# Performance work log

Hardware: AMD Instinct MI355X
Metric: run time of the kernel (lower is better)

The kernel has to match this reference:

```python
import jax, jax.numpy as jnp
import numpy as np

B, NQ, NK = 4, 2048, 2048
D_MODEL, H, DK, DV, M = 512, 8, 64, 64, 40


def setup_inputs() -> dict:
    key = jax.random.key(0)
    ks = jax.random.split(key, 12)
    s = 0.02  # param init scale (stand-in for xavier)
    return {
        "queries": jax.random.normal(ks[0], (B, NQ, D_MODEL), jnp.float32),
        "keys": jax.random.normal(ks[1], (B, NK, D_MODEL), jnp.float32),
        "values": jax.random.normal(ks[2], (B, NK, D_MODEL), jnp.float32),
        "attention_weights": jax.random.uniform(ks[3], (B, H, NQ, NK), jnp.float32),
        "attention_mask": jax.random.randint(ks[4], (B, H, NQ, NK), 0, 2) == 1,
        "Wq": jax.random.normal(ks[5], (D_MODEL, H * DK), jnp.float32) * s,
        "bq": jnp.zeros((H * DK,), jnp.float32),
        "Wk": jax.random.normal(ks[6], (D_MODEL, H * DK), jnp.float32) * s,
        "bk": jnp.zeros((H * DK,), jnp.float32),
        "Wv": jax.random.normal(ks[7], (D_MODEL, H * DV), jnp.float32) * s,
        "bv": jnp.zeros((H * DV,), jnp.float32),
        "Wo": jax.random.normal(ks[8], (H * DV, D_MODEL), jnp.float32) * s,
        "bo": jnp.zeros((D_MODEL,), jnp.float32),
        "m_k": jax.random.normal(ks[9], (1, M, H * DK), jnp.float32) * s,
        "m_v": jax.random.normal(ks[10], (1, M, H * DV), jnp.float32) * s,
    }


def reference(queries, keys, values, attention_weights, attention_mask,
              Wq, bq, Wk, bk, Wv, bv, Wo, bo, m_k, m_v):
    b, nq, _ = queries.shape
    nk = keys.shape[1]
    # learned memory slots, scaled and broadcast over batch
    mk = jnp.sqrt(jnp.float32(DK)) * jnp.broadcast_to(m_k, (b, M, H * DK))
    mv = jnp.sqrt(jnp.float32(M)) * jnp.broadcast_to(m_v, (b, M, H * DV))
    q = (queries @ Wq + bq).reshape(b, nq, H, DK).transpose(0, 2, 1, 3)      # (b,h,nq,dk)
    k = jnp.concatenate([keys @ Wk + bk, mk], axis=1)
    k = k.reshape(b, nk + M, H, DK).transpose(0, 2, 3, 1)                     # (b,h,dk,nk+m)
    v = jnp.concatenate([values @ Wv + bv, mv], axis=1)
    v = v.reshape(b, nk + M, H, DV).transpose(0, 2, 1, 3)                     # (b,h,nk+m,dv)
    att = jnp.matmul(q, k) / jnp.sqrt(jnp.float32(DK))                        # (b,h,nq,nk+m)
    att_x = att[..., :nk] * attention_weights
    att_x = jnp.where(attention_mask, -jnp.inf, att_x)
    att = jnp.concatenate([att_x, att[..., nk:]], axis=-1)
    att = jax.nn.softmax(att, axis=-1)
    out = jnp.matmul(att, v).transpose(0, 2, 1, 3).reshape(b, nq, H * DV)
    return out @ Wo + bo
```

## Files before the change

kernel.cpp:

```cpp
#include <hip/hip_runtime.h>
#include <hip/hip_bf16.h>
#include <cstdint>
#include <cstddef>

typedef __bf16 bf16_t;
typedef __bf16 bf16x8 __attribute__((ext_vector_type(8)));
typedef __bf16 bf16x4 __attribute__((ext_vector_type(4)));
typedef float  f32x4  __attribute__((ext_vector_type(4)));

#define B_    4
#define NQ_   2048
#define NK_   2048
#define H_    8
#define MSL_  40
#define NKP_  2112
#define SCL2  0.18033688011112042f

#define GLOAD_LDS16(GP, LP)                                                        \
    __builtin_amdgcn_global_load_lds(                                              \
        (const __attribute__((address_space(1))) unsigned int*)(GP),               \
        (__attribute__((address_space(3))) unsigned int*)(LP), 16, 0, 0)

__global__ void detect_mask(const unsigned int* __restrict__ m, int* __restrict__ flag)
{
    __shared__ int found;
    if (threadIdx.x == 0) found = 0;
    __syncthreads();
    unsigned int acc = 0;
    for (int i = threadIdx.x; i < 65536; i += 256)
        acc |= (m[i] & 0xFFFFFF00u);
    if (acc) found = 1;
    __syncthreads();
    if (threadIdx.x == 0) *flag = found;
}

__global__ void transpose_convert4(const float* __restrict__ s0, const float* __restrict__ s1,
                                   const float* __restrict__ s2, const float* __restrict__ s3,
                                   bf16_t* __restrict__ d0, bf16_t* __restrict__ d1,
                                   bf16_t* __restrict__ d2, bf16_t* __restrict__ d3)
{
    const float* src; bf16_t* dst;
    switch (blockIdx.z) {
        case 0:  src = s0; dst = d0; break;
        case 1:  src = s1; dst = d1; break;
        case 2:  src = s2; dst = d2; break;
        default: src = s3; dst = d3; break;
    }
    __shared__ float t[32][33];
    int x  = blockIdx.x * 32 + threadIdx.x;
    int y0 = blockIdx.y * 32 + threadIdx.y;
#pragma unroll
    for (int i = 0; i < 32; i += 8)
        t[threadIdx.y + i][threadIdx.x] = src[(size_t)(y0 + i) * 512 + x];
    __syncthreads();
    int ox  = blockIdx.y * 32 + threadIdx.x;
    int oy0 = blockIdx.x * 32 + threadIdx.y;
#pragma unroll
    for (int i = 0; i < 32; i += 8)
        dst[(size_t)(oy0 + i) * 512 + ox] = (bf16_t)t[threadIdx.x][threadIdx.y + i];
}

__global__ void memfill(const float* __restrict__ m_k, const float* __restrict__ m_v,
                        bf16_t* __restrict__ Kbf, bf16_t* __restrict__ Vt)
{
    int tid = blockIdx.x * 256 + threadIdx.x;
    if (tid < 4 * 64 * 512) {
        int c  = tid & 511;
        int mi = (tid >> 9) & 63;
        int b  = tid >> 15;
        float v = (mi < MSL_) ? 8.0f * m_k[mi * 512 + c] : 0.0f;
        Kbf[((size_t)b * NKP_ + NK_ + mi) * 512 + c] = (bf16_t)v;
    } else {
        int t  = tid - 4 * 64 * 512;
        int mi = t & 63;
        int dv = (t >> 6) & 63;
        int h  = (t >> 12) & 7;
        int b  = t >> 15;
        float v = (mi < MSL_) ? 6.324555320336759f * m_v[mi * 512 + h * 64 + dv] : 0.0f;
        Vt[(((size_t)b * H_ + h) * 64 + dv) * NKP_ + NK_ + mi] = (bf16_t)v;
    }
}

template<bool AF32>
__device__ __forceinline__ void gemm_core(
    bf16_t (*As)[72], bf16_t (*Bs)[72],
    const void* __restrict__ Av, const bf16_t* __restrict__ BT,
    const float* __restrict__ bias, void* __restrict__ dstv,
    int dstBS, int epi, float scale)
{
    const int tid = threadIdx.x;
    const int w = tid >> 6, l = tid & 63, lg = l >> 4, lr = l & 15;
    const int wr = w >> 1, wc = w & 1;
    const int blockM = blockIdx.x * 128, blockN = blockIdx.y * 128;

    f32x4 acc[4][4];
    const f32x4 zv = {0.f, 0.f, 0.f, 0.f};
#pragma unroll
    for (int i = 0; i < 4; i++)
#pragma unroll
        for (int j = 0; j < 4; j++) acc[i][j] = zv;

    const int ar = tid >> 1;
    const int ac = (tid & 1) * 32;

    for (int k0 = 0; k0 < 512; k0 += 64) {
        if (k0) __syncthreads();
        if constexpr (AF32) {
            const float* arow = (const float*)Av + (size_t)(blockM + ar) * 512 + k0 + ac;
#pragma unroll
            for (int i = 0; i < 8; i++) {
                float4 v = ((const float4*)arow)[i];
                bf16x4 pk = {(bf16_t)v.x, (bf16_t)v.y, (bf16_t)v.z, (bf16_t)v.w};
                *(bf16x4*)&As[ar][ac + i * 4] = pk;
            }
        } else {
            const bf16_t* arow = (const bf16_t*)Av + (size_t)(blockM + ar) * 512 + k0 + ac;
#pragma unroll
            for (int i = 0; i < 4; i++)
                *(uint4*)&As[ar][ac + i * 8] = ((const uint4*)arow)[i];
        }
        {
            const bf16_t* brow = BT + (size_t)(blockN + ar) * 512 + k0 + ac;
#pragma unroll
            for (int i = 0; i < 4; i++)
                *(uint4*)&Bs[ar][ac + i * 8] = ((const uint4*)brow)[i];
        }
        __syncthreads();
#pragma unroll
        for (int ks = 0; ks < 2; ks++) {
            bf16x8 af[4], bfr[4];
#pragma unroll
            for (int mi = 0; mi < 4; mi++)
                af[mi] = *(const bf16x8*)&As[wr * 64 + mi * 16 + lr][ks * 32 + lg * 8];
#pragma unroll
            for (int ni = 0; ni < 4; ni++)
                bfr[ni] = *(const bf16x8*)&Bs[wc * 64 + ni * 16 + lr][ks * 32 + lg * 8];
#pragma unroll
            for (int mi = 0; mi < 4; mi++)
#pragma unroll
                for (int ni = 0; ni < 4; ni++)
                    acc[mi][ni] = __builtin_amdgcn_mfma_f32_16x16x32_bf16(af[mi], bfr[ni], acc[mi][ni], 0, 0, 0);
        }
    }

    const int colbase = blockN + wc * 64;
    float bias_v[4];
#pragma unroll
    for (int ni = 0; ni < 4; ni++) bias_v[ni] = bias[colbase + ni * 16 + lr];

#pragma unroll
    for (int mi = 0; mi < 4; mi++) {
        const int r0 = blockM + wr * 64 + mi * 16 + lg * 4;
#pragma unroll
        for (int ni = 0; ni < 4; ni++) {
            const int c = colbase + ni * 16 + lr;
            f32x4 v = acc[mi][ni];
            if (epi == 2) {
                float* dst = (float*)dstv;
#pragma unroll
                for (int j = 0; j < 4; j++)
                    dst[(size_t)(r0 + j) * 512 + c] = (v[j] + bias_v[ni]) * scale;
            } else if (epi == 0) {
                bf16_t* dst = (bf16_t*)dstv;
#pragma unroll
                for (int j = 0; j < 4; j++) {
                    int rr = r0 + j;
                    int bb = rr >> 11, nn = rr & 2047;
                    dst[((size_t)bb * dstBS + nn) * 512 + c] = (bf16_t)((v[j] + bias_v[ni]) * scale);
                }
            } else {
                bf16_t* dst = (bf16_t*)dstv;
                int bb = r0 >> 11, n0 = r0 & 2047;
                int hh = c >> 6, dv = c & 63;
                bf16x4 pk;
#pragma unroll
                for (int j = 0; j < 4; j++) pk[j] = (bf16_t)((v[j] + bias_v[ni]) * scale);
                *(bf16x4*)(dst + (((size_t)bb * H_ + hh) * 64 + dv) * NKP_ + n0) = pk;
            }
        }
    }
}

__global__ __launch_bounds__(256) void gemm_qkv(
    const float* __restrict__ q, const float* __restrict__ k, const float* __restrict__ v,
    const bf16_t* __restrict__ WqT, const bf16_t* __restrict__ WkT, const bf16_t* __restrict__ WvT,
    const float* __restrict__ bq, const float* __restrict__ bk, const float* __restrict__ bv,
    bf16_t* __restrict__ Qbf, bf16_t* __restrict__ Kbf, bf16_t* __restrict__ Vt)
{
    __shared__ bf16_t As[128][72];
    __shared__ bf16_t Bs[128][72];
    const void* Av; const bf16_t* BT; const float* bias; void* dst;
    int dstBS, epi; float scale = 1.0f;
    switch (blockIdx.z) {
        case 0:  Av = q; BT = WqT; bias = bq; dst = Qbf; dstBS = 2048; epi = 0; scale = SCL2; break;
        case 1:  Av = k; BT = WkT; bias = bk; dst = Kbf; dstBS = NKP_; epi = 0; break;
        default: Av = v; BT = WvT; bias = bv; dst = Vt;  dstBS = 0;    epi = 1; break;
    }
    gemm_core<true>(As, Bs, Av, BT, bias, dst, dstBS, epi, scale);
}

__global__ __launch_bounds__(256) void gemm_fin(
    const bf16_t* __restrict__ Obuf, const bf16_t* __restrict__ WoT,
    const float* __restrict__ bo, float* __restrict__ out)
{
    __shared__ bf16_t As[128][72];
    __shared__ bf16_t Bs[128][72];
    gemm_core<false>(As, Bs, Obuf, WoT, bo, out, 0, 2, 1.0f);
}

template<bool BYTEM>
__global__ __launch_bounds__(256) void attn_fused(
    const bf16_t* __restrict__ Qbf, const bf16_t* __restrict__ Kbf,
    const bf16_t* __restrict__ Vt, const float* __restrict__ attw,
    const void* __restrict__ maskv, const int* __restrict__ mflag,
    bf16_t* __restrict__ Obuf)
{
    if ((*mflag != 0) != BYTEM) return;

    __shared__ bf16_t Ks[2][64][64];
    __shared__ bf16_t Vs[2][64][64];
    __shared__ bf16_t Pl[4][1024];

    const int tid = threadIdx.x;
    const int wv = tid >> 6, l = tid & 63, lg = l >> 4, lr = l & 15;
    const int qt = blockIdx.x, h = blockIdx.y, b = blockIdx.z;
    const int q0w = qt * 64 + wv * 16;
    bf16_t* Pw = &Pl[wv][0];

    const size_t bh = (size_t)(b * H_ + h);
    const float* wbase = attw + bh * (size_t)NQ_ * NK_;
    const unsigned char* mb8 = (const unsigned char*)maskv + bh * (size_t)NQ_ * NK_;
    const int* mb32 = (const int*)maskv + bh * (size_t)NQ_ * NK_;
    const char* kbase8 = (const char*)(Kbf + (size_t)b * NKP_ * 512 + h * 64);
    const char* vbase8 = (const char*)(Vt + bh * 64 * (size_t)NKP_);

    bf16x8 qf0 = *(const bf16x8*)&Qbf[((size_t)b * NQ_ + q0w + lr) * 512 + h * 64 + lg * 8];
    bf16x8 qf1 = *(const bf16x8*)&Qbf[((size_t)b * NQ_ + q0w + lr) * 512 + h * 64 + 32 + lg * 8];

    const f32x4 zv = {0.f, 0.f, 0.f, 0.f};
    f32x4 oacc[4];
#pragma unroll
    for (int i = 0; i < 4; i++) oacc[i] = zv;
    float lsum = 0.f;
    f32x4 sA[4];

    f32x4 wA[4], wB[4];
    unsigned mA[4], mB[4];
    unsigned miA[16], miB[16];

    const int srow = l >> 3;
    const int scsw = ((l & 7) ^ (srow & 7)) * 16;

#define STAGE(BUF, KCB) do {                                                      \
    _Pragma("unroll") for (int pi_ = 0; pi_ < 2; pi_++) {                         \
        const int p_ = wv * 2 + pi_;                                              \
        const int r_ = p_ * 8 + srow;                                             \
        GLOAD_LDS16(kbase8 + (size_t)((KCB) + r_) * 1024 + scsw,                  \
                    (char*)&Ks[BUF][0][0] + p_ * 1024);                           \
        GLOAD_LDS16(vbase8 + (size_t)r_ * 4224 + (size_t)(KCB) * 2 + scsw,        \
                    (char*)&Vs[BUF][0][0] + p_ * 1024);                           \
    }                                                                             \
} while (0)

#define PREFETCH(KT, WB_, MB_, MIB_) do {                                         \
    const float* wp_ = wbase + (size_t)(q0w + lr) * NK_ + (KT) * 64 + lg * 4;     \
    _Pragma("unroll") for (int n_ = 0; n_ < 4; n_++)                              \
        WB_[n_] = *(const f32x4*)(wp_ + n_ * 16);                                 \
    if constexpr (BYTEM) {                                                        \
        const unsigned char* mp_ = mb8 + (size_t)(q0w + lr) * NK_ + (KT) * 64 + lg * 4; \
        _Pragma("unroll") for (int n_ = 0; n_ < 4; n_++)                          \
            MB_[n_] = *(const unsigned*)(mp_ + n_ * 16);                          \
    } else {                                                                      \
        const int* mp_ = mb32 + (size_t)(q0w + lr) * NK_ + (KT) * 64 + lg * 4;    \
        _Pragma("unroll") for (int n_ = 0; n_ < 4; n_++) {                        \
            uint4 t_ = *(const uint4*)(mp_ + n_ * 16);                            \
            MIB_[n_ * 4 + 0] = t_.x; MIB_[n_ * 4 + 1] = t_.y;                     \
            MIB_[n_ * 4 + 2] = t_.z; MIB_[n_ * 4 + 3] = t_.w; }                   \
    }                                                                             \
} while (0)

#define QKT_LDS(BC) do {                                                          \
    const int sw_ = (lg ^ (lr & 7)) * 8;                                          \
    _Pragma("unroll") for (int n_ = 0; n_ < 4; n_++) {                            \
        const int kr_ = n_ * 16 + lr;                                             \
        f32x4 a_ = zv;                                                            \
        a_ = __builtin_amdgcn_mfma_f32_16x16x32_bf16(*(const bf16x8*)&Ks[BC][kr_][sw_], qf0, a_, 0, 0, 0); \
        a_ = __builtin_amdgcn_mfma_f32_16x16x32_bf16(*(const bf16x8*)&Ks[BC][kr_][sw_ ^ 32], qf1, a_, 0, 0, 0); \
        sA[n_] = a_;                                                              \
    }                                                                             \
} while (0)

#define APPLY(WB_, MB_, MIB_) do {                                                \
    _Pragma("unroll") for (int n_ = 0; n_ < 4; n_++)                              \
    _Pragma("unroll") for (int j_ = 0; j_ < 4; j_++) {                            \
        bool mk_;                                                                 \
        if constexpr (BYTEM) mk_ = ((MB_[n_] >> (8 * j_)) & 0xffu) != 0;          \
        else                 mk_ = (MIB_[n_ * 4 + j_] != 0);                      \
        sA[n_][j_] = mk_ ? -1e30f : sA[n_][j_] * WB_[n_][j_];                     \
    }                                                                             \
} while (0)

#define SMPV(BC) do {                                                             \
    _Pragma("unroll") for (int n_ = 0; n_ < 4; n_++)                              \
    _Pragma("unroll") for (int j_ = 0; j_ < 4; j_++) {                            \
        float p_ = exp2f(sA[n_][j_]);                                             \
        sA[n_][j_] = p_; lsum += p_;                                              \
    }                                                                             \
    _Pragma("unroll") for (int n_ = 0; n_ < 4; n_++) {                            \
        int c_ = n_ * 2 + (lg >> 1);                                              \
        int qp_ = (lr + 4 * c_) & 15;                                             \
        bf16x4 pk_ = {(bf16_t)sA[n_][0], (bf16_t)sA[n_][1],                       \
                      (bf16_t)sA[n_][2], (bf16_t)sA[n_][3]};                      \
        *(bf16x4*)&Pw[c_ * 128 + qp_ * 8 + (lg & 1) * 4] = pk_;                   \
    }                                                                             \
    bf16x8 pf0_ = *(const bf16x8*)&Pw[lg * 128 + ((lr + 4 * lg) & 15) * 8];       \
    bf16x8 pf1_ = *(const bf16x8*)&Pw[(4 + lg) * 128 + ((lr + 4 * (4 + lg)) & 15) * 8]; \
    const int vsw_ = (lg ^ (lr & 7)) * 8;                                         \
    _Pragma("unroll") for (int n2_ = 0; n2_ < 4; n2_++) {                         \
        const int vr_ = n2_ * 16 + lr;                                            \
        oacc[n2_] = __builtin_amdgcn_mfma_f32_16x16x32_bf16(*(const bf16x8*)&Vs[BC][vr_][vsw_], pf0_, oacc[n2_], 0, 0, 0); \
        oacc[n2_] = __builtin_amdgcn_mfma_f32_16x16x32_bf16(*(const bf16x8*)&Vs[BC][vr_][vsw_ ^ 32], pf1_, oacc[n2_], 0, 0, 0); \
    }                                                                             \
} while (0)

#define BODYT(KT, BC, BN, WB_, MB_, MIB_, WN_, MN_, MIN_) do {                    \
    if ((KT) < 31) STAGE(BN, ((KT) + 1) * 64);                                    \
    QKT_LDS(BC);                                                                  \
    if ((KT) < 31) PREFETCH((KT) + 1, WN_, MN_, MIN_);                            \
    APPLY(WB_, MB_, MIB_);                                                        \
    SMPV(BC);                                                                     \
    __syncthreads();                                                              \
} while (0)

    STAGE(0, 2048);
    PREFETCH(0, wA, mA, miA);
    __syncthreads();

    {
        STAGE(1, 0);
        QKT_LDS(0);
#pragma unroll
        for (int n_ = 0; n_ < 4; n_++)
#pragma unroll
            for (int j_ = 0; j_ < 4; j_++) {
                int kloc = n_ * 16 + lg * 4 + j_;
                sA[n_][j_] = (kloc >= MSL_) ? -1e30f : sA[n_][j_];
            }
        SMPV(0);
        __syncthreads();
    }

    for (int kt = 0; kt < 32; kt += 2) {
        BODYT(kt,     1, 0, wA, mA, miA, wB, mB, miB);
        BODYT(kt + 1, 0, 1, wB, mB, miB, wA, mA, miA);
    }

    float ts = lsum;
    ts += __shfl_xor(ts, 16);
    ts += __shfl_xor(ts, 32);
    float invl = 1.0f / ts;
#pragma unroll
    for (int n2 = 0; n2 < 4; n2++) {
        bf16x4 ov = {(bf16_t)(oacc[n2][0] * invl), (bf16_t)(oacc[n2][1] * invl),
                     (bf16_t)(oacc[n2][2] * invl), (bf16_t)(oacc[n2][3] * invl)};
        *(bf16x4*)&Obuf[((size_t)b * NQ_ + q0w + lr) * 512 + h * 64 + n2 * 16 + lg * 4] = ov;
    }

#undef STAGE
#undef PREFETCH
#undef QKT_LDS
#undef APPLY
#undef SMPV
#undef BODYT
}

extern "C" void kernel_launch(void* const* d_in, const int* in_sizes, int n_in,
                              void* d_out, int out_size, void* d_ws, size_t ws_size,
                              hipStream_t stream)
{
    const float* queries = (const float*)d_in[0];
    const float* keys    = (const float*)d_in[1];
    const float* values  = (const float*)d_in[2];
    const float* attw    = (const float*)d_in[3];
    const void*  maskv   = d_in[4];
    const float* Wq = (const float*)d_in[5];
    const float* bq = (const float*)d_in[6];
    const float* Wk = (const float*)d_in[7];
    const float* bk = (const float*)d_in[8];
    const float* Wv = (const float*)d_in[9];
    const float* bv = (const float*)d_in[10];
    const float* Wo = (const float*)d_in[11];
    const float* bo = (const float*)d_in[12];
    const float* m_k = (const float*)d_in[13];
    const float* m_v = (const float*)d_in[14];

    char* ws = (char*)d_ws;
    bf16_t* WqT  = (bf16_t*)(ws + 0);
    bf16_t* WkT  = (bf16_t*)(ws + 524288);
    bf16_t* WvT  = (bf16_t*)(ws + 1048576);
    bf16_t* WoT  = (bf16_t*)(ws + 1572864);
    bf16_t* Qbf  = (bf16_t*)(ws + 2097152);
    bf16_t* Kbf  = (bf16_t*)(ws + 10485760);
    bf16_t* Vt   = (bf16_t*)(ws + 19136512);
    bf16_t* Obuf = (bf16_t*)(ws + 27787264);
    int*    mflag = (int*)(ws + 36175872);

    detect_mask<<<1, 256, 0, stream>>>((const unsigned int*)maskv, mflag);
    transpose_convert4<<<dim3(16, 16, 4), dim3(32, 8), 0, stream>>>(
        Wq, Wk, Wv, Wo, WqT, WkT, WvT, WoT);
    memfill<<<1024, 256, 0, stream>>>(m_k, m_v, Kbf, Vt);

    gemm_qkv<<<dim3(64, 4, 3), 256, 0, stream>>>(
        queries, keys, values, WqT, WkT, WvT, bq, bk, bv, Qbf, Kbf, Vt);

    attn_fused<true><<<dim3(32, H_, B_), 256, 0, stream>>>(Qbf, Kbf, Vt, attw, maskv, mflag, Obuf);
    attn_fused<false><<<dim3(32, H_, B_), 256, 0, stream>>>(Qbf, Kbf, Vt, attw, maskv, mflag, Obuf);

    gemm_fin<<<dim3(64, 4), 256, 0, stream>>>(Obuf, WoT, bo, (float*)d_out);
    (void)in_sizes; (void)n_in; (void)out_size; (void)ws_size;
}
```

Measured before the change: 394.9 us.

## Load K/V tiles directly into registers instead of staging through LDS

Removes the shared-memory double buffers for K and V and the per-tile __syncthreads; each wave now loads its K and V MFMA operands straight from global memory into registers, with the next tile loaded while the current one is computed. The attention-weight and mask prefetch is moved two tiles ahead instead of one. This drops LDS traffic and block-wide barriers, but every wave now reads the same K/V data separately (4x redundant global/L2 traffic) and holds many more live registers, which may lower occupancy.

```diff
diff --git a/kernel.cpp b/kernel.cpp
--- a/kernel.cpp
+++ b/kernel.cpp
@@ -15,11 +15,6 @@
 #define MSL_  40
 #define NKP_  2112
 #define SCL2  0.18033688011112042f
-
-#define GLOAD_LDS16(GP, LP)                                                        \
-    __builtin_amdgcn_global_load_lds(                                              \
-        (const __attribute__((address_space(1))) unsigned int*)(GP),               \
-        (__attribute__((address_space(3))) unsigned int*)(LP), 16, 0, 0)
 
 __global__ void detect_mask(const unsigned int* __restrict__ m, int* __restrict__ flag)
 {
@@ -217,8 +212,6 @@
 {
     if ((*mflag != 0) != BYTEM) return;
 
-    __shared__ bf16_t Ks[2][64][64];
-    __shared__ bf16_t Vs[2][64][64];
     __shared__ bf16_t Pl[4][1024];
 
     const int tid = threadIdx.x;
@@ -231,8 +224,8 @@
     const float* wbase = attw + bh * (size_t)NQ_ * NK_;
     const unsigned char* mb8 = (const unsigned char*)maskv + bh * (size_t)NQ_ * NK_;
     const int* mb32 = (const int*)maskv + bh * (size_t)NQ_ * NK_;
-    const char* kbase8 = (const char*)(Kbf + (size_t)b * NKP_ * 512 + h * 64);
-    const char* vbase8 = (const char*)(Vt + bh * 64 * (size_t)NKP_);
+    const bf16_t* kbase = Kbf + (size_t)b * NKP_ * 512 + h * 64;
+    const bf16_t* vbase = Vt + bh * 64 * (size_t)NKP_;
 
     bf16x8 qf0 = *(const bf16x8*)&Qbf[((size_t)b * NQ_ + q0w + lr) * 512 + h * 64 + lg * 8];
     bf16x8 qf1 = *(const bf16x8*)&Qbf[((size_t)b * NQ_ + q0w + lr) * 512 + h * 64 + 32 + lg * 8];
@@ -244,21 +237,25 @@
     float lsum = 0.f;
     f32x4 sA[4];
 
+    bf16x8 kf[8];
+    bf16x8 vf[8];
     f32x4 wA[4], wB[4];
     unsigned mA[4], mB[4];
     unsigned miA[16], miB[16];
 
-    const int srow = l >> 3;
-    const int scsw = ((l & 7) ^ (srow & 7)) * 16;
-
-#define STAGE(BUF, KCB) do {                                                      \
-    _Pragma("unroll") for (int pi_ = 0; pi_ < 2; pi_++) {                         \
-        const int p_ = wv * 2 + pi_;                                              \
-        const int r_ = p_ * 8 + srow;                                             \
-        GLOAD_LDS16(kbase8 + (size_t)((KCB) + r_) * 1024 + scsw,                  \
-                    (char*)&Ks[BUF][0][0] + p_ * 1024);                           \
-        GLOAD_LDS16(vbase8 + (size_t)r_ * 4224 + (size_t)(KCB) * 2 + scsw,        \
-                    (char*)&Vs[BUF][0][0] + p_ * 1024);                           \
+#define KLOAD(KCB) do {                                                           \
+    _Pragma("unroll") for (int n_ = 0; n_ < 4; n_++) {                            \
+        const bf16_t* kp_ = kbase + (size_t)((KCB) + n_ * 16 + lr) * 512 + lg * 8;\
+        kf[n_ * 2]     = *(const bf16x8*)kp_;                                     \
+        kf[n_ * 2 + 1] = *(const bf16x8*)(kp_ + 32);                              \
+    }                                                                             \
+} while (0)
+
+#define VLOAD(KCB) do {                                                           \
+    _Pragma("unroll") for (int n_ = 0; n_ < 4; n_++) {                            \
+        const bf16_t* vp_ = vbase + (size_t)(n_ * 16 + lr) * NKP_ + (KCB) + lg * 8; \
+        vf[n_ * 2]     = *(const bf16x8*)vp_;                                     \
+        vf[n_ * 2 + 1] = *(const bf16x8*)(vp_ + 32);                              \
     }                                                                             \
 } while (0)
 
@@ -279,13 +276,11 @@
     }                                                                             \
 } while (0)
 
-#define QKT_LDS(BC) do {                                                          \
-    const int sw_ = (lg ^ (lr & 7)) * 8;                                          \
+#define QKT_R() do {                                                              \
     _Pragma("unroll") for (int n_ = 0; n_ < 4; n_++) {                            \
-        const int kr_ = n_ * 16 + lr;                                             \
         f32x4 a_ = zv;                                                            \
-        a_ = __builtin_amdgcn_mfma_f32_16x16x32_bf16(*(const bf16x8*)&Ks[BC][kr_][sw_], qf0, a_, 0, 0, 0); \
-        a_ = __builtin_amdgcn_mfma_f32_16x16x32_bf16(*(const bf16x8*)&Ks[BC][kr_][sw_ ^ 32], qf1, a_, 0, 0, 0); \
+        a_ = __builtin_amdgcn_mfma_f32_16x16x32_bf16(kf[n_ * 2],     qf0, a_, 0, 0, 0); \
+        a_ = __builtin_amdgcn_mfma_f32_16x16x32_bf16(kf[n_ * 2 + 1], qf1, a_, 0, 0, 0); \
         sA[n_] = a_;                                                              \
     }                                                                             \
 } while (0)
@@ -300,7 +295,7 @@
     }                                                                             \
 } while (0)
 
-#define SMPV(BC) do {                                                             \
+#define SMPV_R() do {                                                             \
     _Pragma("unroll") for (int n_ = 0; n_ < 4; n_++)                              \
     _Pragma("unroll") for (int j_ = 0; j_ < 4; j_++) {                            \
         float p_ = exp2f(sA[n_][j_]);                                             \
@@ -315,30 +310,28 @@
     }                                                                             \
     bf16x8 pf0_ = *(const bf16x8*)&Pw[lg * 128 + ((lr + 4 * lg) & 15) * 8];       \
     bf16x8 pf1_ = *(const bf16x8*)&Pw[(4 + lg) * 128 + ((lr + 4 * (4 + lg)) & 15) * 8]; \
-    const int vsw_ = (lg ^ (lr & 7)) * 8;                                         \
     _Pragma("unroll") for (int n2_ = 0; n2_ < 4; n2_++) {                         \
-        const int vr_ = n2_ * 16 + lr;                                            \
-        oacc[n2_] = __builtin_amdgcn_mfma_f32_16x16x32_bf16(*(const bf16x8*)&Vs[BC][vr_][vsw_], pf0_, oacc[n2_], 0, 0, 0); \
-        oacc[n2_] = __builtin_amdgcn_mfma_f32_16x16x32_bf16(*(const bf16x8*)&Vs[BC][vr_][vsw_ ^ 32], pf1_, oacc[n2_], 0, 0, 0); \
-    }                                                                             \
-} while (0)
-
-#define BODYT(KT, BC, BN, WB_, MB_, MIB_, WN_, MN_, MIN_) do {                    \
-    if ((KT) < 31) STAGE(BN, ((KT) + 1) * 64);                                    \
-    QKT_LDS(BC);                                                                  \
-    if ((KT) < 31) PREFETCH((KT) + 1, WN_, MN_, MIN_);                            \
-    APPLY(WB_, MB_, MIB_);                                                        \
-    SMPV(BC);                                                                     \
-    __syncthreads();                                                              \
-} while (0)
-
-    STAGE(0, 2048);
+        oacc[n2_] = __builtin_amdgcn_mfma_f32_16x16x32_bf16(vf[n2_ * 2],     pf0_, oacc[n2_], 0, 0, 0); \
+        oacc[n2_] = __builtin_amdgcn_mfma_f32_16x16x32_bf16(vf[n2_ * 2 + 1], pf1_, oacc[n2_], 0, 0, 0); \
+    }                                                                             \
+} while (0)
+
+#define BODY(T, WC_, MC_, MIC_) do {                                              \
+    QKT_R();                                                                      \
+    if ((T) < 31) KLOAD(((T) + 1) * 64);                                          \
+    APPLY(WC_, MC_, MIC_);                                                        \
+    if ((T) < 30) PREFETCH((T) + 2, WC_, MC_, MIC_);                              \
+    SMPV_R();                                                                     \
+    if ((T) < 31) VLOAD(((T) + 1) * 64);                                          \
+} while (0)
+
+    KLOAD(2048);
+    VLOAD(2048);
     PREFETCH(0, wA, mA, miA);
-    __syncthreads();
 
     {
-        STAGE(1, 0);
-        QKT_LDS(0);
+        QKT_R();
+        KLOAD(0);
 #pragma unroll
         for (int n_ = 0; n_ < 4; n_++)
 #pragma unroll
@@ -346,13 +339,14 @@
                 int kloc = n_ * 16 + lg * 4 + j_;
                 sA[n_][j_] = (kloc >= MSL_) ? -1e30f : sA[n_][j_];
             }
-        SMPV(0);
-        __syncthreads();
-    }
-
-    for (int kt = 0; kt < 32; kt += 2) {
-        BODYT(kt,     1, 0, wA, mA, miA, wB, mB, miB);
-        BODYT(kt + 1, 0, 1, wB, mB, miB, wA, mA, miA);
+        PREFETCH(1, wB, mB, miB);
+        SMPV_R();
+        VLOAD(0);
+    }
+
+    for (int t = 0; t < 32; t += 2) {
+        BODY(t,     wA, mA, miA);
+        BODY(t + 1, wB, mB, miB);
     }
 
     float ts = lsum;
@@ -366,12 +360,13 @@
         *(bf16x4*)&Obuf[((size_t)b * NQ_ + q0w + lr) * 512 + h * 64 + n2 * 16 + lg * 4] = ov;
     }
 
-#undef STAGE
+#undef KLOAD
+#undef VLOAD
 #undef PREFETCH
-#undef QKT_LDS
+#undef QKT_R
 #undef APPLY
-#undef SMPV
-#undef BODYT
+#undef SMPV_R
+#undef BODY
 }
 
 extern "C" void kernel_launch(void* const* d_in, const int* in_sizes, int n_in,
```

Result: slower. 501.9 us (+27.1%).
